# Performance work log

Hardware: AMD Instinct MI355X
Metric: run time of the kernel (lower is better)

## Reference

```python
import jax, jax.numpy as jnp
import numpy as np

N_NODES = 50000
N_EDGES = 800000
EMB = 96
LAYER_NUM = 3


def setup_inputs() -> dict:
    key = jax.random.key(0)
    k1, k2, k3, k4 = jax.random.split(key, 4)
    X = jax.random.normal(k1, (N_NODES, EMB), dtype=jnp.float32)
    vals = jax.random.uniform(k2, (N_EDGES,), dtype=jnp.float32)
    rows = jax.random.randint(k3, (N_EDGES,), 0, N_NODES, dtype=jnp.int64)
    cols = jax.random.randint(k4, (N_EDGES,), 0, N_NODES, dtype=jnp.int64)
    return {"X": X, "vals": vals, "rows": rows, "cols": cols}


def reference(X, vals, rows, cols):
    # Eval-mode GNN forward: dropout layers are identity, graph is not dropped.
    # Per layer: agg = A @ ego  (COO SpMM via gather + segment_sum), then
    # ego = agg + agg * ego (elementwise gating). Output = mean over all layers.
    N = X.shape[0]
    ego = X
    acc = X  # running sum of layer embeddings (layer 0 = X)
    for _ in range(LAYER_NUM):
        # SpMM: gather source features, scale by edge values, scatter-add to rows
        msgs = vals[:, None] * ego[cols]          # [E, D]
        agg = jax.ops.segment_sum(msgs, rows, num_segments=N)  # [N, D]
        ego = agg + agg * ego
        acc = acc + ego
    return acc / jnp.asarray(LAYER_NUM + 1, dtype=X.dtype)
```

## Files before the change

kernel.cpp:

```cpp
#include <hip/hip_runtime.h>
#include <hip/hip_bf16.h>


#define N_NODES 50000
#define N_EDGES 800000
#define EMB 96
#define C16 12
#define TPR 6
#define LAYER_NUM 3
#define PAD 64
#define NCHUNK (N_NODES * C16)

#define NBUCK 196
#define RPB 256
#define CAP 5000
#define EDGE_BLOCKS 782
#define CONV_BLOCKS 2344

__device__ __forceinline__ float bflo(unsigned u) { return __uint_as_float(u << 16); }
__device__ __forceinline__ float bfhi(unsigned u) { return __uint_as_float(u & 0xffff0000u); }

__device__ __forceinline__ void fma_bf8(float* s, float v, const uint4& u) {
    s[0] = fmaf(v, bflo(u.x), s[0]);
    s[1] = fmaf(v, bfhi(u.x), s[1]);
    s[2] = fmaf(v, bflo(u.y), s[2]);
    s[3] = fmaf(v, bfhi(u.y), s[3]);
    s[4] = fmaf(v, bflo(u.z), s[4]);
    s[5] = fmaf(v, bfhi(u.z), s[5]);
    s[6] = fmaf(v, bflo(u.w), s[6]);
    s[7] = fmaf(v, bfhi(u.w), s[7]);
}

__device__ __forceinline__ void unpack8(float* d, const uint4& u) {
    d[0] = bflo(u.x); d[1] = bfhi(u.x);
    d[2] = bflo(u.y); d[3] = bfhi(u.y);
    d[4] = bflo(u.z); d[5] = bfhi(u.z);
    d[6] = bflo(u.w); d[7] = bfhi(u.w);
}

__device__ __forceinline__ unsigned packbf(float a, float b) {
    unsigned ua = __float_as_uint(a);
    unsigned ub = __float_as_uint(b);
    ua = (ua + 0x7fffu + ((ua >> 16) & 1u)) >> 16;
    ub = (ub + 0x7fffu + ((ub >> 16) & 1u)) & 0xffff0000u;
    return ua | ub;
}

__global__ void setup_kernel(const float4* __restrict__ X4,
                             uint4* __restrict__ Xb,
                             const int4* __restrict__ rows4,
                             const int4* __restrict__ cols4,
                             const float4* __restrict__ vals4,
                             int* __restrict__ bucket_cnt,
                             uint2* __restrict__ bucket_buf) {
    __shared__ int hist[NBUCK];
    __shared__ int gbase[NBUCK];
    int tid = threadIdx.x;

    if (blockIdx.x < EDGE_BLOCKS) {
        for (int i = tid; i < NBUCK; i += 256) hist[i] = 0;
        __syncthreads();

        int e = blockIdx.x * 256 + tid;
        bool act = (e < N_EDGES / 4);
        int4 r, c; float4 v;
        int b0 = 0, b1 = 0, b2 = 0, b3 = 0;
        int k0 = 0, k1 = 0, k2 = 0, k3 = 0;
        if (act) {
            r = rows4[e]; c = cols4[e]; v = vals4[e];
            b0 = r.x >> 8; b1 = r.y >> 8; b2 = r.z >> 8; b3 = r.w >> 8;
            k0 = atomicAdd(&hist[b0], 1);
            k1 = atomicAdd(&hist[b1], 1);
            k2 = atomicAdd(&hist[b2], 1);
            k3 = atomicAdd(&hist[b3], 1);
        }
        __syncthreads();

        for (int i = tid; i < NBUCK; i += 256)
            gbase[i] = atomicAdd(&bucket_cnt[i], hist[i]);
        __syncthreads();

        if (act) {
            uint2 p;
            int d;
            d = gbase[b0] + k0;
            if (d < CAP) {
                p.x = (unsigned)c.x | ((unsigned)(r.x & 255) << 24);
                p.y = __float_as_uint(v.x);
                bucket_buf[b0 * CAP + d] = p;
            }
            d = gbase[b1] + k1;
            if (d < CAP) {
                p.x = (unsigned)c.y | ((unsigned)(r.y & 255) << 24);
                p.y = __float_as_uint(v.y);
                bucket_buf[b1 * CAP + d] = p;
            }
            d = gbase[b2] + k2;
            if (d < CAP) {
                p.x = (unsigned)c.z | ((unsigned)(r.z & 255) << 24);
                p.y = __float_as_uint(v.z);
                bucket_buf[b2 * CAP + d] = p;
            }
            d = gbase[b3] + k3;
            if (d < CAP) {
                p.x = (unsigned)c.w | ((unsigned)(r.w & 255) << 24);
                p.y = __float_as_uint(v.w);
                bucket_buf[b3 * CAP + d] = p;
            }
        }
    } else {
        int chunk = (blockIdx.x - EDGE_BLOCKS) * 256 + tid;
        if (chunk < NCHUNK) {
            float4 a = X4[chunk * 2];
            float4 b = X4[chunk * 2 + 1];
            uint4 o;
            o.x = packbf(a.x, a.y);
            o.y = packbf(a.z, a.w);
            o.z = packbf(b.x, b.y);
            o.w = packbf(b.z, b.w);
            Xb[chunk] = o;
        }
    }
}

__global__ void ell_build_kernel(const int* __restrict__ bucket_cnt,
                                 const uint2* __restrict__ bucket_buf,
                                 int2* __restrict__ ell,
                                 int* __restrict__ cnt) {
    __shared__ int lc[RPB];
    int b = blockIdx.x;
    int tid = threadIdx.x;
    if (tid < RPB) lc[tid] = 0;
    __syncthreads();

    int n = bucket_cnt[b];
    if (n > CAP) n = CAP;
    const uint2* buf = bucket_buf + b * CAP;
    for (int i = tid; i < n; i += 512) {
        uint2 rec = buf[i];
        int rl = rec.x >> 24;
        int slot = atomicAdd(&lc[rl], 1);
        if (slot < PAD) {
            int2 p;
            p.x = (int)(rec.x & 0x00ffffffu);
            p.y = (int)rec.y;
            ell[(b * RPB + rl) * PAD + slot] = p;
        }
    }
    __syncthreads();
    if (tid < RPB) {
        int row = b * RPB + tid;
        if (row < N_NODES) {
            int d = lc[tid];
            cnt[row] = (d > PAD) ? PAD : d;
        }
    }
}

template <int MODE>
__global__ void spmm_fused_kernel(const uint4* __restrict__ ego_in,
                                  uint4* __restrict__ ego_out,
                                  const int* __restrict__ cnt,
                                  const int4* __restrict__ ell4,
                                  const uint4* __restrict__ xb,
                                  const uint4* __restrict__ e1v,
                                  float4* __restrict__ acc) {
    int tid = blockIdx.x * blockDim.x + threadIdx.x;
    if (tid >= N_NODES * TPR) return;
    int row = tid / TPR;
    int ct  = tid % TPR;

    int deg = cnt[row];
    const int4* ep = ell4 + row * (PAD / 2);

    float s0[8] = {0.f, 0.f, 0.f, 0.f, 0.f, 0.f, 0.f, 0.f};
    float s1[8] = {0.f, 0.f, 0.f, 0.f, 0.f, 0.f, 0.f, 0.f};

    int j = 0;
    for (; j + 4 <= deg; j += 4) {
        int4 pA = ep[j >> 1];
        int4 pB = ep[(j >> 1) + 1];
        const uint4* b0 = ego_in + pA.x * C16;
        const uint4* b1 = ego_in + pA.z * C16;
        const uint4* b2 = ego_in + pB.x * C16;
        const uint4* b3 = ego_in + pB.z * C16;
        uint4 x0a = b0[ct], x0b = b0[ct + TPR];
        uint4 x1a = b1[ct], x1b = b1[ct + TPR];
        uint4 x2a = b2[ct], x2b = b2[ct + TPR];
        uint4 x3a = b3[ct], x3b = b3[ct + TPR];
        float v0 = __int_as_float(pA.y);
        float v1 = __int_as_float(pA.w);
        float v2 = __int_as_float(pB.y);
        float v3 = __int_as_float(pB.w);
        fma_bf8(s0, v0, x0a); fma_bf8(s1, v0, x0b);
        fma_bf8(s0, v1, x1a); fma_bf8(s1, v1, x1b);
        fma_bf8(s0, v2, x2a); fma_bf8(s1, v2, x2b);
        fma_bf8(s0, v3, x3a); fma_bf8(s1, v3, x3b);
    }
    for (; j + 2 <= deg; j += 2) {
        int4 pA = ep[j >> 1];
        const uint4* b0 = ego_in + pA.x * C16;
        const uint4* b1 = ego_in + pA.z * C16;
        uint4 x0a = b0[ct], x0b = b0[ct + TPR];
        uint4 x1a = b1[ct], x1b = b1[ct + TPR];
        float v0 = __int_as_float(pA.y);
        float v1 = __int_as_float(pA.w);
        fma_bf8(s0, v0, x0a); fma_bf8(s1, v0, x0b);
        fma_bf8(s0, v1, x1a); fma_bf8(s1, v1, x1b);
    }
    if (j < deg) {
        int2 p = ((const int2*)ell4)[row * PAD + j];
        const uint4* b0 = ego_in + p.x * C16;
        uint4 x0a = b0[ct], x0b = b0[ct + TPR];
        float v0 = __int_as_float(p.y);
        fma_bf8(s0, v0, x0a); fma_bf8(s1, v0, x0b);
    }

    int ib = row * C16 + ct;
    uint4 ea = ego_in[ib];
    uint4 eb = ego_in[ib + TPR];
    float e0[8], e1[8];
    unpack8(e0, ea);
    unpack8(e1, eb);
    float n0[8], n1[8];
#pragma unroll
    for (int k = 0; k < 8; ++k) {
        n0[k] = fmaf(s0[k], e0[k], s0[k]);
        n1[k] = fmaf(s1[k], e1[k], s1[k]);
    }

    if (MODE == 0) {
        uint4 oa, ob;
        oa.x = packbf(n0[0], n0[1]); oa.y = packbf(n0[2], n0[3]);
        oa.z = packbf(n0[4], n0[5]); oa.w = packbf(n0[6], n0[7]);
        ob.x = packbf(n1[0], n1[1]); ob.y = packbf(n1[2], n1[3]);
        ob.z = packbf(n1[4], n1[5]); ob.w = packbf(n1[6], n1[7]);
        ego_out[ib]       = oa;
        ego_out[ib + TPR] = ob;
    } else {
        float x0[8], x1[8], f0[8], f1[8];
        unpack8(x0, xb[ib]);
        unpack8(x1, xb[ib + TPR]);
        unpack8(f0, e1v[ib]);
        unpack8(f1, e1v[ib + TPR]);
        int ia = row * (EMB / 4) + ct * 2;
        float4 a0, a1, a2, a3;
        a0.x = (x0[0] + f0[0] + e0[0] + n0[0]) * 0.25f;
        a0.y = (x0[1] + f0[1] + e0[1] + n0[1]) * 0.25f;
        a0.z = (x0[2] + f0[2] + e0[2] + n0[2]) * 0.25f;
        a0.w = (x0[3] + f0[3] + e0[3] + n0[3]) * 0.25f;
        a1.x = (x0[4] + f0[4] + e0[4] + n0[4]) * 0.25f;
        a1.y = (x0[5] + f0[5] + e0[5] + n0[5]) * 0.25f;
        a1.z = (x0[6] + f0[6] + e0[6] + n0[6]) * 0.25f;
        a1.w = (x0[7] + f0[7] + e0[7] + n0[7]) * 0.25f;
        a2.x = (x1[0] + f1[0] + e1[0] + n1[0]) * 0.25f;
        a2.y = (x1[1] + f1[1] + e1[1] + n1[1]) * 0.25f;
        a2.z = (x1[2] + f1[2] + e1[2] + n1[2]) * 0.25f;
        a2.w = (x1[3] + f1[3] + e1[3] + n1[3]) * 0.25f;
        a3.x = (x1[4] + f1[4] + e1[4] + n1[4]) * 0.25f;
        a3.y = (x1[5] + f1[5] + e1[5] + n1[5]) * 0.25f;
        a3.z = (x1[6] + f1[6] + e1[6] + n1[6]) * 0.25f;
        a3.w = (x1[7] + f1[7] + e1[7] + n1[7]) * 0.25f;
        acc[ia]      = a0;
        acc[ia + 1]  = a1;
        acc[ia + 12] = a2;
        acc[ia + 13] = a3;
    }
}

extern "C" void kernel_launch(void* const* d_in, const int* in_sizes, int n_in,
                              void* d_out, int out_size, void* d_ws, size_t ws_size,
                              hipStream_t stream) {
    const float* X    = (const float*)d_in[0];
    const float* vals = (const float*)d_in[1];
    const int*   rows = (const int*)d_in[2];
    const int*   cols = (const int*)d_in[3];

    const size_t nodeb_bytes = (size_t)NCHUNK * sizeof(uint4);
    const size_t ell_bytes   = (size_t)N_NODES * PAD * sizeof(int2);
    const size_t cnt_bytes   = (size_t)N_NODES * sizeof(int);

    float* acc = (float*)d_out;

    char* w = (char*)d_ws;
    uint4* Xb    = (uint4*)w;  w += nodeb_bytes;
    uint4* ego_a = (uint4*)w;  w += nodeb_bytes;
    uint4* ego_b = (uint4*)w;  w += nodeb_bytes;
    int2*  ell   = (int2*)w;   w += ell_bytes;
    int*   cnt   = (int*)w;    w += cnt_bytes;

    uint2* bucket_buf = (uint2*)ego_a;
    int*   bucket_cnt = (int*)ego_b;

    hipMemsetAsync(bucket_cnt, 0, NBUCK * sizeof(int), stream);

    setup_kernel<<<EDGE_BLOCKS + CONV_BLOCKS, 256, 0, stream>>>(
        (const float4*)X, Xb,
        (const int4*)rows, (const int4*)cols, (const float4*)vals,
        bucket_cnt, bucket_buf);

    ell_build_kernel<<<NBUCK, 512, 0, stream>>>(bucket_cnt, bucket_buf, ell, cnt);

    const int blocks = (N_NODES * TPR + 255) / 256;

    spmm_fused_kernel<0><<<blocks, 256, 0, stream>>>(
        Xb, ego_a, cnt, (const int4*)ell, nullptr, nullptr, nullptr);
    spmm_fused_kernel<0><<<blocks, 256, 0, stream>>>(
        ego_a, ego_b, cnt, (const int4*)ell, nullptr, nullptr, nullptr);
    spmm_fused_kernel<1><<<blocks, 256, 0, stream>>>(
        ego_b, nullptr, cnt, (const int4*)ell, Xb, ego_a, (float4*)acc);
}
```

Baseline: 190.1 us.

## Split embeddings into column-slice planes and run SpMM per slice

Stores bf16 node embeddings as three 32-column planes and launches the fused SpMM/gating kernel once per slice, with 4 threads per row. This shrinks the randomly gathered working set per launch so gathers can hit in L2 more often. In exchange, the ELL index and degree arrays are re-read once per slice, and the launch count triples.

```diff
diff --git a/kernel.cpp b/kernel.cpp
--- a/kernel.cpp
+++ b/kernel.cpp
@@ -6,10 +6,11 @@
 #define N_EDGES 800000
 #define EMB 96
 #define C16 12
-#define TPR 6
 #define LAYER_NUM 3
 #define PAD 64
 #define NCHUNK (N_NODES * C16)
+#define NSLICE 3
+#define PLANE_U4 (N_NODES * 4)
 
 #define NBUCK 196
 #define RPB 256
@@ -118,7 +119,9 @@
             o.y = packbf(a.z, a.w);
             o.z = packbf(b.x, b.y);
             o.w = packbf(b.z, b.w);
-            Xb[chunk] = o;
+            int row = chunk / C16;
+            int ct  = chunk % C16;
+            Xb[(ct >> 2) * PLANE_U4 + row * 4 + (ct & 3)] = o;
         }
     }
 }
@@ -158,93 +161,78 @@
 }
 
 template <int MODE>
-__global__ void spmm_fused_kernel(const uint4* __restrict__ ego_in,
+__global__ void spmm_slice_kernel(const uint4* __restrict__ ego_in,
                                   uint4* __restrict__ ego_out,
                                   const int* __restrict__ cnt,
                                   const int4* __restrict__ ell4,
                                   const uint4* __restrict__ xb,
                                   const uint4* __restrict__ e1v,
-                                  float4* __restrict__ acc) {
+                                  float4* __restrict__ acc,
+                                  int slice) {
     int tid = blockIdx.x * blockDim.x + threadIdx.x;
-    if (tid >= N_NODES * TPR) return;
-    int row = tid / TPR;
-    int ct  = tid % TPR;
+    if (tid >= N_NODES * 4) return;
+    int row = tid >> 2;
+    int q   = tid & 3;
+
+    const uint4* in_pl = ego_in + slice * PLANE_U4;
 
     int deg = cnt[row];
     const int4* ep = ell4 + row * (PAD / 2);
 
     float s0[8] = {0.f, 0.f, 0.f, 0.f, 0.f, 0.f, 0.f, 0.f};
-    float s1[8] = {0.f, 0.f, 0.f, 0.f, 0.f, 0.f, 0.f, 0.f};
 
     int j = 0;
     for (; j + 4 <= deg; j += 4) {
         int4 pA = ep[j >> 1];
         int4 pB = ep[(j >> 1) + 1];
-        const uint4* b0 = ego_in + pA.x * C16;
-        const uint4* b1 = ego_in + pA.z * C16;
-        const uint4* b2 = ego_in + pB.x * C16;
-        const uint4* b3 = ego_in + pB.z * C16;
-        uint4 x0a = b0[ct], x0b = b0[ct + TPR];
-        uint4 x1a = b1[ct], x1b = b1[ct + TPR];
-        uint4 x2a = b2[ct], x2b = b2[ct + TPR];
-        uint4 x3a = b3[ct], x3b = b3[ct + TPR];
+        uint4 x0 = in_pl[(pA.x << 2) + q];
+        uint4 x1 = in_pl[(pA.z << 2) + q];
+        uint4 x2 = in_pl[(pB.x << 2) + q];
+        uint4 x3 = in_pl[(pB.z << 2) + q];
         float v0 = __int_as_float(pA.y);
         float v1 = __int_as_float(pA.w);
         float v2 = __int_as_float(pB.y);
         float v3 = __int_as_float(pB.w);
-        fma_bf8(s0, v0, x0a); fma_bf8(s1, v0, x0b);
-        fma_bf8(s0, v1, x1a); fma_bf8(s1, v1, x1b);
-        fma_bf8(s0, v2, x2a); fma_bf8(s1, v2, x2b);
-        fma_bf8(s0, v3, x3a); fma_bf8(s1, v3, x3b);
+        fma_bf8(s0, v0, x0);
+        fma_bf8(s0, v1, x1);
+        fma_bf8(s0, v2, x2);
+        fma_bf8(s0, v3, x3);
     }
     for (; j + 2 <= deg; j += 2) {
         int4 pA = ep[j >> 1];
-        const uint4* b0 = ego_in + pA.x * C16;
-        const uint4* b1 = ego_in + pA.z * C16;
-        uint4 x0a = b0[ct], x0b = b0[ct + TPR];
-        uint4 x1a = b1[ct], x1b = b1[ct + TPR];
+        uint4 x0 = in_pl[(pA.x << 2) + q];
+        uint4 x1 = in_pl[(pA.z << 2) + q];
         float v0 = __int_as_float(pA.y);
         float v1 = __int_as_float(pA.w);
-        fma_bf8(s0, v0, x0a); fma_bf8(s1, v0, x0b);
-        fma_bf8(s0, v1, x1a); fma_bf8(s1, v1, x1b);
+        fma_bf8(s0, v0, x0);
+        fma_bf8(s0, v1, x1);
     }
     if (j < deg) {
         int2 p = ((const int2*)ell4)[row * PAD + j];
-        const uint4* b0 = ego_in + p.x * C16;
-        uint4 x0a = b0[ct], x0b = b0[ct + TPR];
+        uint4 x0 = in_pl[(p.x << 2) + q];
         float v0 = __int_as_float(p.y);
-        fma_bf8(s0, v0, x0a); fma_bf8(s1, v0, x0b);
-    }
-
-    int ib = row * C16 + ct;
-    uint4 ea = ego_in[ib];
-    uint4 eb = ego_in[ib + TPR];
-    float e0[8], e1[8];
-    unpack8(e0, ea);
-    unpack8(e1, eb);
-    float n0[8], n1[8];
+        fma_bf8(s0, v0, x0);
+    }
+
+    int ib = (row << 2) + q;
+    float e0[8];
+    unpack8(e0, in_pl[ib]);
+    float n0[8];
 #pragma unroll
-    for (int k = 0; k < 8; ++k) {
+    for (int k = 0; k < 8; ++k)
         n0[k] = fmaf(s0[k], e0[k], s0[k]);
-        n1[k] = fmaf(s1[k], e1[k], s1[k]);
-    }
 
     if (MODE == 0) {
-        uint4 oa, ob;
+        uint4 oa;
         oa.x = packbf(n0[0], n0[1]); oa.y = packbf(n0[2], n0[3]);
         oa.z = packbf(n0[4], n0[5]); oa.w = packbf(n0[6], n0[7]);
-        ob.x = packbf(n1[0], n1[1]); ob.y = packbf(n1[2], n1[3]);
-        ob.z = packbf(n1[4], n1[5]); ob.w = packbf(n1[6], n1[7]);
-        ego_out[ib]       = oa;
-        ego_out[ib + TPR] = ob;
+        ego_out[slice * PLANE_U4 + ib] = oa;
     } else {
-        float x0[8], x1[8], f0[8], f1[8];
-        unpack8(x0, xb[ib]);
-        unpack8(x1, xb[ib + TPR]);
-        unpack8(f0, e1v[ib]);
-        unpack8(f1, e1v[ib + TPR]);
-        int ia = row * (EMB / 4) + ct * 2;
-        float4 a0, a1, a2, a3;
+        float x0[8], f0[8];
+        unpack8(x0, xb[slice * PLANE_U4 + ib]);
+        unpack8(f0, e1v[slice * PLANE_U4 + ib]);
+        int ia = row * (EMB / 4) + slice * 8 + q * 2;
+        float4 a0, a1;
         a0.x = (x0[0] + f0[0] + e0[0] + n0[0]) * 0.25f;
         a0.y = (x0[1] + f0[1] + e0[1] + n0[1]) * 0.25f;
         a0.z = (x0[2] + f0[2] + e0[2] + n0[2]) * 0.25f;
@@ -253,18 +241,8 @@
         a1.y = (x0[5] + f0[5] + e0[5] + n0[5]) * 0.25f;
         a1.z = (x0[6] + f0[6] + e0[6] + n0[6]) * 0.25f;
         a1.w = (x0[7] + f0[7] + e0[7] + n0[7]) * 0.25f;
-        a2.x = (x1[0] + f1[0] + e1[0] + n1[0]) * 0.25f;
-        a2.y = (x1[1] + f1[1] + e1[1] + n1[1]) * 0.25f;
-        a2.z = (x1[2] + f1[2] + e1[2] + n1[2]) * 0.25f;
-        a2.w = (x1[3] + f1[3] + e1[3] + n1[3]) * 0.25f;
-        a3.x = (x1[4] + f1[4] + e1[4] + n1[4]) * 0.25f;
-        a3.y = (x1[5] + f1[5] + e1[5] + n1[5]) * 0.25f;
-        a3.z = (x1[6] + f1[6] + e1[6] + n1[6]) * 0.25f;
-        a3.w = (x1[7] + f1[7] + e1[7] + n1[7]) * 0.25f;
-        acc[ia]      = a0;
-        acc[ia + 1]  = a1;
-        acc[ia + 12] = a2;
-        acc[ia + 13] = a3;
+        acc[ia]     = a0;
+        acc[ia + 1] = a1;
     }
 }
 
@@ -301,12 +279,15 @@
 
     ell_build_kernel<<<NBUCK, 512, 0, stream>>>(bucket_cnt, bucket_buf, ell, cnt);
 
-    const int blocks = (N_NODES * TPR + 255) / 256;
-
-    spmm_fused_kernel<0><<<blocks, 256, 0, stream>>>(
-        Xb, ego_a, cnt, (const int4*)ell, nullptr, nullptr, nullptr);
-    spmm_fused_kernel<0><<<blocks, 256, 0, stream>>>(
-        ego_a, ego_b, cnt, (const int4*)ell, nullptr, nullptr, nullptr);
-    spmm_fused_kernel<1><<<blocks, 256, 0, stream>>>(
-        ego_b, nullptr, cnt, (const int4*)ell, Xb, ego_a, (float4*)acc);
-}
+    const int blocks = (N_NODES * 4 + 255) / 256;
+
+    for (int s = 0; s < NSLICE; ++s)
+        spmm_slice_kernel<0><<<blocks, 256, 0, stream>>>(
+            Xb, ego_a, cnt, (const int4*)ell, nullptr, nullptr, nullptr, s);
+    for (int s = 0; s < NSLICE; ++s)
+        spmm_slice_kernel<0><<<blocks, 256, 0, stream>>>(
+            ego_a, ego_b, cnt, (const int4*)ell, nullptr, nullptr, nullptr, s);
+    for (int s = 0; s < NSLICE; ++s)
+        spmm_slice_kernel<1><<<blocks, 256, 0, stream>>>(
+            ego_b, nullptr, cnt, (const int4*)ell, Xb, ego_a, (float4*)acc, s);
+}
```

Result: slower. 220.9 us (+16.2%).
